# Kernel tuning notes

Measured on AMD Instinct MI355X. Metric: run time of the kernel, lower is better.

Reference implementation:

```python
import jax, jax.numpy as jnp
import numpy as np

N_NODES = 100000
N_EDGES = 1600000
D = 32  # atom and bond feature dim


def _mlp(x, W1, b1, W2, b2, W3, b3):
    # fff: Linear(in,128) -> ReLU -> Linear(128,64) -> ReLU -> Linear(64,32)
    h = jax.nn.relu(x @ W1 + b1)
    h = jax.nn.relu(h @ W2 + b2)
    return h @ W3 + b3


def _init_mlp(key, in_dim):
    ks = jax.random.split(key, 3)
    def lin(k, fan_in, fan_out):
        bound = 1.0 / np.sqrt(fan_in)
        kw, kb = jax.random.split(k)
        W = jax.random.uniform(kw, (fan_in, fan_out), jnp.float32, -bound, bound)
        b = jax.random.uniform(kb, (fan_out,), jnp.float32, -bound, bound)
        return W, b
    W1, b1 = lin(ks[0], in_dim, 128)
    W2, b2 = lin(ks[1], 128, 64)
    W3, b3 = lin(ks[2], 64, 32)
    return W1, b1, W2, b2, W3, b3


def setup_inputs() -> dict:
    key = jax.random.key(0)
    k_bonds, k_a1, k_a2, k_atoms, k_e, k_v = jax.random.split(key, 6)
    inp = {
        "bonds": jax.random.normal(k_bonds, (N_EDGES, D), jnp.float32),
        "bond_atom_1": jax.random.randint(k_a1, (N_EDGES,), 0, N_NODES, jnp.int64),
        "bond_atom_2": jax.random.randint(k_a2, (N_EDGES,), 0, N_NODES, jnp.int64),
        "atoms": jax.random.normal(k_atoms, (N_NODES, D), jnp.float32),
    }
    We1, be1, We2, be2, We3, be3 = _init_mlp(k_e, 96)
    Wv1, bv1, Wv2, bv2, Wv3, bv3 = _init_mlp(k_v, 64)
    inp.update(We1=We1, be1=be1, We2=We2, be2=be2, We3=We3, be3=be3,
               Wv1=Wv1, bv1=bv1, Wv2=Wv2, bv2=bv2, Wv3=Wv3, bv3=bv3)
    return inp


def reference(bonds, bond_atom_1, bond_atom_2, atoms,
              We1, be1, We2, be2, We3, be3,
              Wv1, bv1, Wv2, bv2, Wv3, bv3):
    # Edge update: gather endpoint atom features, concat with bond feats, MLP
    atom1 = atoms[bond_atom_1]                    # [E, D]
    atom2 = atoms[bond_atom_2]                    # [E, D]
    e_in = jnp.concatenate([atom1, atom2, bonds], axis=1)  # [E, 3D]
    new_bonds = _mlp(e_in, We1, be1, We2, be2, We3, be3)    # [E, 32]

    # Node update: scatter-mean new bond features onto target atoms
    # (PyG default flow aggregates messages at edge_index[1] == bond_atom_2)
    n = atoms.shape[0]
    seg_sum = jax.ops.segment_sum(new_bonds, bond_atom_2, num_segments=n)
    counts = jax.ops.segment_sum(jnp.ones((new_bonds.shape[0],), new_bonds.dtype),
                                 bond_atom_2, num_segments=n)
    mean_bonds = seg_sum / jnp.maximum(counts, 1.0)[:, None]  # [N, 32]

    v_in = jnp.concatenate([mean_bonds, atoms], axis=1)        # [N, 64]
    new_atoms = _mlp(v_in, Wv1, bv1, Wv2, bv2, Wv3, bv3)       # [N, 32]
    return (new_atoms, new_bonds)
```

## Files before the change

kernel.cpp:

```cpp
#include <hip/hip_runtime.h>
#include <hip/hip_bf16.h>

#define NN 100000
#define NE 1600000
#define NB_SCAN 391
#define ETILES 12500
#define EGRID 512
#define NGRID 1024

typedef __attribute__((ext_vector_type(8))) short bfrag8;
typedef __attribute__((ext_vector_type(4))) float f32x4;
typedef __attribute__((ext_vector_type(8))) unsigned short us8;
typedef __attribute__((ext_vector_type(4))) unsigned int u32x4;

__device__ __forceinline__ unsigned short f2bf(float f) {
  unsigned int u = __float_as_uint(f);
  u += 0x7fffu + ((u >> 16) & 1u);
  return (unsigned short)(u >> 16);
}

__device__ __forceinline__ unsigned int pk2(float a, float b) {
  unsigned int r;
  asm("v_cvt_pk_bf16_f32 %0, %1, %2" : "=v"(r) : "v"(a), "v"(b));
  return r;
}

__device__ __forceinline__ uint2 pk4(float v0, float v1, float v2, float v3) {
  return make_uint2(pk2(v0, v1), pk2(v2, v3));
}

__device__ __forceinline__ bfrag8 pack8(float4 a, float4 b) {
  union { u32x4 u; bfrag8 f; } c;
  c.u[0] = pk2(a.x, a.y); c.u[1] = pk2(a.z, a.w);
  c.u[2] = pk2(b.x, b.y); c.u[3] = pk2(b.z, b.w);
  return c.f;
}

__device__ __forceinline__ bfrag8 as_frag(us8 v) {
  union { us8 u; bfrag8 f; } c;
  c.u = v;
  return c.f;
}

__device__ __forceinline__ f32x4 mfma16(bfrag8 a, bfrag8 b, f32x4 c) {
  return __builtin_amdgcn_mfma_f32_16x16x32_bf16(a, b, c, 0, 0, 0);
}

__device__ __forceinline__ void gload_lds16(const void* g, void* l) {
  __builtin_amdgcn_global_load_lds(
      (const __attribute__((address_space(1))) unsigned int*)g,
      (__attribute__((address_space(3))) unsigned int*)l, 16, 0, 0);
}

__global__ void cvt_atoms(const float* __restrict__ src, unsigned short* __restrict__ dst) {
  int i = blockIdx.x * 256 + threadIdx.x;
  float4 v = *(const float4*)(src + (size_t)i * 4);
  *(uint2*)(dst + (size_t)i * 4) = pk4(v.x, v.y, v.z, v.w);
}

__global__ void pack_w(const float* __restrict__ src, unsigned short* __restrict__ dst,
                       int K, int N) {
  int i = blockIdx.x * 256 + threadIdx.x;
  if (i >= K * N) return;
  int j = i & 7;
  int gc = i >> 3;
  int c = gc % N;
  int g = gc / N;
  dst[i] = f2bf(src[(g * 8 + j) * N + c]);
}

__global__ void count_k(const int* __restrict__ a2, int* __restrict__ cnt) {
  int e = blockIdx.x * 256 + threadIdx.x;
  if (e < NE) atomicAdd(&cnt[a2[e]], 1);
}

__global__ void scan_blocks(const int* __restrict__ cnt, int* __restrict__ off,
                            int* __restrict__ bsum) {
  __shared__ int s[256];
  const int t = threadIdx.x;
  const int idx = blockIdx.x * 256 + t;
  int v = (idx < NN) ? cnt[idx] : 0;
  s[t] = v;
  __syncthreads();
  for (int d = 1; d < 256; d <<= 1) {
    int x = (t >= d) ? s[t - d] : 0;
    __syncthreads();
    s[t] += x;
    __syncthreads();
  }
  if (idx < NN) off[idx] = s[t] - v;
  if (t == 255) bsum[blockIdx.x] = s[255];
}

__global__ void scan_bsum(int* __restrict__ bsum) {
  __shared__ int s[512];
  const int t = threadIdx.x;
  int v = (t < NB_SCAN) ? bsum[t] : 0;
  s[t] = v;
  __syncthreads();
  for (int d = 1; d < 512; d <<= 1) {
    int x = (t >= d) ? s[t - d] : 0;
    __syncthreads();
    s[t] += x;
    __syncthreads();
  }
  if (t < NB_SCAN) bsum[t] = s[t] - v;
}

__global__ void scan_finalize(int* __restrict__ off, const int* __restrict__ bsum,
                              int* __restrict__ cursor) {
  int idx = blockIdx.x * 256 + threadIdx.x;
  if (idx < NN) {
    int o = off[idx] + bsum[blockIdx.x];
    off[idx] = o;
    cursor[idx] = o;
  }
  if (idx == 0) off[NN] = NE;
}

__global__ void fill_csr(const int* __restrict__ a2, int* __restrict__ cursor,
                         int* __restrict__ csr) {
  int e = blockIdx.x * 256 + threadIdx.x;
  if (e < NE) {
    int p = atomicAdd(&cursor[a2[e]], 1);
    csr[p] = e;
  }
}

__global__ __launch_bounds__(256, 2) void edge_kernel(
    const float* __restrict__ bonds, const int* __restrict__ a1p, const int* __restrict__ a2p,
    const unsigned short* __restrict__ atoms_bf,
    const float* __restrict__ be1, const float* __restrict__ be2, const float* __restrict__ be3,
    const unsigned short* __restrict__ wpack,
    float* __restrict__ new_bonds) {
  __shared__ unsigned short sW[22528];
  __shared__ float sB1[128], sB2[64], sB3[32];
  __shared__ unsigned short sH1[128 * 136];

  const int tid = threadIdx.x;
  const int lane = tid & 63, wv = tid >> 6;
  const int cl = lane & 15, q = lane >> 4;
  const int esub = wv * 32 + cl;

  {
    const char* src = (const char*)wpack;
    char* dst = (char*)sW;
#pragma unroll
    for (int i = 0; i < 11; ++i) {
      const int c = i * 4 + wv;
      gload_lds16(src + c * 1024 + lane * 16, dst + c * 1024);
    }
  }
  if (tid < 128) sB1[tid] = be1[tid];
  else if (tid < 192) sB2[tid - 128] = be2[tid - 128];
  else if (tid < 224) sB3[tid - 192] = be3[tid - 192];

  int tile = blockIdx.x;
  us8 ra1[2], ra2[2];
  float4 rb[2][2];
  int ia1n[2], ia2n[2];

#pragma unroll
  for (int t = 0; t < 2; ++t) {
    const int e = tile * 128 + esub + t * 16;
    const int ia1 = a1p[e], ia2 = a2p[e];
    ra1[t] = *(const us8*)(atoms_bf + (size_t)ia1 * 32 + q * 8);
    ra2[t] = *(const us8*)(atoms_bf + (size_t)ia2 * 32 + q * 8);
    const float* bp = bonds + (size_t)e * 32 + q * 8;
    rb[t][0] = *(const float4*)(bp);
    rb[t][1] = *(const float4*)(bp + 4);
  }
  {
    int tn = tile + EGRID; if (tn >= ETILES) tn = tile;
#pragma unroll
    for (int t = 0; t < 2; ++t) {
      const int e = tn * 128 + esub + t * 16;
      ia1n[t] = a1p[e]; ia2n[t] = a2p[e];
    }
  }
  __syncthreads();

  for (; tile < ETILES; tile += EGRID) {
    bfrag8 xb0[2], xb1[2], xb2[2];
#pragma unroll
    for (int t = 0; t < 2; ++t) {
      xb0[t] = as_frag(ra1[t]);
      xb1[t] = as_frag(ra2[t]);
      xb2[t] = pack8(rb[t][0], rb[t][1]);
    }
    const int tn = (tile + EGRID < ETILES) ? tile + EGRID : tile;
#pragma unroll
    for (int t = 0; t < 2; ++t) {
      ra1[t] = *(const us8*)(atoms_bf + (size_t)ia1n[t] * 32 + q * 8);
      ra2[t] = *(const us8*)(atoms_bf + (size_t)ia2n[t] * 32 + q * 8);
      const int e = tn * 128 + esub + t * 16;
      const float* bp = bonds + (size_t)e * 32 + q * 8;
      rb[t][0] = *(const float4*)(bp);
      rb[t][1] = *(const float4*)(bp + 4);
    }
    {
      int tnn = tile + 2 * EGRID; if (tnn >= ETILES) tnn = tn;
#pragma unroll
      for (int t = 0; t < 2; ++t) {
        const int e = tnn * 128 + esub + t * 16;
        ia1n[t] = a1p[e]; ia2n[t] = a2p[e];
      }
    }

#pragma unroll
    for (int rt = 0; rt < 8; ++rt) {
      const unsigned short* wa = &sW[(q * 128 + rt * 16 + cl) * 8];
      bfrag8 w0 = *(const bfrag8*)(wa);
      bfrag8 w1 = *(const bfrag8*)(wa + 4096);
      bfrag8 w2 = *(const bfrag8*)(wa + 8192);
      f32x4 acc[2];
      acc[0] = (f32x4){0.f, 0.f, 0.f, 0.f};
      acc[1] = (f32x4){0.f, 0.f, 0.f, 0.f};
#pragma unroll
      for (int t = 0; t < 2; ++t) {
        acc[t] = mfma16(w0, xb0[t], acc[t]);
        acc[t] = mfma16(w1, xb1[t], acc[t]);
        acc[t] = mfma16(w2, xb2[t], acc[t]);
      }
      const int c0 = rt * 16 + q * 4;
#pragma unroll
      for (int t = 0; t < 2; ++t) {
        uint2 hv = pk4(fmaxf(acc[t][0] + sB1[c0 + 0], 0.f),
                       fmaxf(acc[t][1] + sB1[c0 + 1], 0.f),
                       fmaxf(acc[t][2] + sB1[c0 + 2], 0.f),
                       fmaxf(acc[t][3] + sB1[c0 + 3], 0.f));
        *(uint2*)&sH1[(esub + t * 16) * 136 + c0] = hv;
      }
    }
    __syncthreads();

    bfrag8 hb[4][2];
#pragma unroll
    for (int t = 0; t < 2; ++t) {
      const unsigned short* hr = &sH1[(esub + t * 16) * 136 + q * 8];
#pragma unroll
      for (int ks = 0; ks < 4; ++ks) hb[ks][t] = *(const bfrag8*)(hr + ks * 32);
    }
    __syncthreads();

    unsigned short* sH2 = sH1;
#pragma unroll
    for (int rt = 0; rt < 4; ++rt) {
      f32x4 acc[2];
      acc[0] = (f32x4){0.f, 0.f, 0.f, 0.f};
      acc[1] = (f32x4){0.f, 0.f, 0.f, 0.f};
#pragma unroll
      for (int ks = 0; ks < 4; ++ks) {
        bfrag8 w = *(const bfrag8*)&sW[12288 + ks * 2048 + (q * 64 + rt * 16 + cl) * 8];
#pragma unroll
        for (int t = 0; t < 2; ++t) acc[t] = mfma16(w, hb[ks][t], acc[t]);
      }
      const int c0 = rt * 16 + q * 4;
#pragma unroll
      for (int t = 0; t < 2; ++t) {
        uint2 hv = pk4(fmaxf(acc[t][0] + sB2[c0 + 0], 0.f),
                       fmaxf(acc[t][1] + sB2[c0 + 1], 0.f),
                       fmaxf(acc[t][2] + sB2[c0 + 2], 0.f),
                       fmaxf(acc[t][3] + sB2[c0 + 3], 0.f));
        *(uint2*)&sH2[(esub + t * 16) * 72 + c0] = hv;
      }
    }
    __syncthreads();

    bfrag8 gb0[2], gb1[2];
#pragma unroll
    for (int t = 0; t < 2; ++t) {
      const unsigned short* hr = &sH2[(esub + t * 16) * 72 + q * 8];
      gb0[t] = *(const bfrag8*)(hr);
      gb1[t] = *(const bfrag8*)(hr + 32);
    }
#pragma unroll
    for (int rt = 0; rt < 2; ++rt) {
      bfrag8 w0 = *(const bfrag8*)&sW[20480 + (q * 32 + rt * 16 + cl) * 8];
      bfrag8 w1 = *(const bfrag8*)&sW[20480 + 1024 + (q * 32 + rt * 16 + cl) * 8];
      const int c0 = rt * 16 + q * 4;
#pragma unroll
      for (int t = 0; t < 2; ++t) {
        f32x4 acc = {0.f, 0.f, 0.f, 0.f};
        acc = mfma16(w0, gb0[t], acc);
        acc = mfma16(w1, gb1[t], acc);
        const int e = tile * 128 + esub + t * 16;
        float4 o;
        o.x = acc[0] + sB3[c0 + 0];
        o.y = acc[1] + sB3[c0 + 1];
        o.z = acc[2] + sB3[c0 + 2];
        o.w = acc[3] + sB3[c0 + 3];
        *(float4*)(new_bonds + (size_t)e * 32 + c0) = o;
      }
    }
    __syncthreads();
  }
}

__global__ __launch_bounds__(256, 4) void gather_mean(
    const int* __restrict__ off, const int* __restrict__ csr,
    const float* __restrict__ new_bonds, float* __restrict__ mean_f32) {
  const int tid = blockIdx.x * 256 + threadIdx.x;
  const int n = tid >> 3, sl = tid & 7;
  const int o0 = off[n], o1 = off[n + 1];
  float4 s0 = {0.f, 0.f, 0.f, 0.f}, s1 = {0.f, 0.f, 0.f, 0.f};
  int i = o0;
  for (; i + 1 < o1; i += 2) {
    const int ea = csr[i], eb = csr[i + 1];
    float4 a = *(const float4*)(new_bonds + (size_t)ea * 32 + sl * 4);
    float4 b = *(const float4*)(new_bonds + (size_t)eb * 32 + sl * 4);
    s0.x += a.x; s0.y += a.y; s0.z += a.z; s0.w += a.w;
    s1.x += b.x; s1.y += b.y; s1.z += b.z; s1.w += b.w;
  }
  if (i < o1) {
    const int ea = csr[i];
    float4 a = *(const float4*)(new_bonds + (size_t)ea * 32 + sl * 4);
    s0.x += a.x; s0.y += a.y; s0.z += a.z; s0.w += a.w;
  }
  const float inv = 1.0f / fmaxf((float)(o1 - o0), 1.0f);
  float4 m;
  m.x = (s0.x + s1.x) * inv;
  m.y = (s0.y + s1.y) * inv;
  m.z = (s0.z + s1.z) * inv;
  m.w = (s0.w + s1.w) * inv;
  *(float4*)(mean_f32 + (size_t)n * 32 + sl * 4) = m;
}

__global__ __launch_bounds__(256, 4) void node_mlp(
    const unsigned short* __restrict__ atoms_bf,
    const float* __restrict__ bv1, const float* __restrict__ bv2, const float* __restrict__ bv3,
    const unsigned short* __restrict__ wpack,
    const float* __restrict__ mean_f32, float* __restrict__ new_atoms) {
  __shared__ unsigned short sW[18432];
  __shared__ float sB1[128], sB2[64], sB3[32];
  __shared__ unsigned short sV[64 * 72];
  __shared__ unsigned short sH1[64 * 136];

  const int tid = threadIdx.x;
  const int lane = tid & 63, wv = tid >> 6;
  const int cl = lane & 15, q = lane >> 4;
  const int nl = tid >> 2, l4 = tid & 3;

  {
    const uint4* src = (const uint4*)wpack;
    uint4* dst = (uint4*)sW;
#pragma unroll
    for (int i = 0; i < 9; ++i) dst[tid + i * 256] = src[tid + i * 256];
  }
  if (tid < 128) sB1[tid] = bv1[tid];
  if (tid < 64) sB2[tid] = bv2[tid];
  if (tid < 32) sB3[tid] = bv3[tid];

  for (int n0 = blockIdx.x * 64; n0 < NN; n0 += NGRID * 64) {
    __syncthreads();

    {
      const int n = n0 + nl;
      if (n < NN) {
        if (l4 < 2) {
          const float* sp = mean_f32 + (size_t)n * 32 + l4 * 16;
          float4 a = *(const float4*)(sp);
          float4 b = *(const float4*)(sp + 4);
          float4 c = *(const float4*)(sp + 8);
          float4 d = *(const float4*)(sp + 12);
          uint4 o0, o1;
          o0.x = pk2(a.x, a.y); o0.y = pk2(a.z, a.w);
          o0.z = pk2(b.x, b.y); o0.w = pk2(b.z, b.w);
          o1.x = pk2(c.x, c.y); o1.y = pk2(c.z, c.w);
          o1.z = pk2(d.x, d.y); o1.w = pk2(d.z, d.w);
          *(uint4*)&sV[nl * 72 + l4 * 16] = o0;
          *(uint4*)&sV[nl * 72 + l4 * 16 + 8] = o1;
        } else {
          const unsigned short* ap = atoms_bf + (size_t)n * 32 + (l4 - 2) * 16;
          *(us8*)&sV[nl * 72 + 32 + (l4 - 2) * 16] = *(const us8*)(ap);
          *(us8*)&sV[nl * 72 + 32 + (l4 - 2) * 16 + 8] = *(const us8*)(ap + 8);
        }
      } else {
        us8 z = {0, 0, 0, 0, 0, 0, 0, 0};
        *(us8*)&sV[nl * 72 + l4 * 16] = z;
        *(us8*)&sV[nl * 72 + l4 * 16 + 8] = z;
      }
    }
    __syncthreads();

    const int nt = wv * 16;
    const int ng = n0 + nt + cl;

    bfrag8 vb0 = *(const bfrag8*)&sV[(nt + cl) * 72 + q * 8];
    bfrag8 vb1 = *(const bfrag8*)&sV[(nt + cl) * 72 + 32 + q * 8];
#pragma unroll
    for (int rt = 0; rt < 8; ++rt) {
      f32x4 acc = {0.f, 0.f, 0.f, 0.f};
      acc = mfma16(*(const bfrag8*)&sW[(q * 128 + rt * 16 + cl) * 8], vb0, acc);
      acc = mfma16(*(const bfrag8*)&sW[4096 + (q * 128 + rt * 16 + cl) * 8], vb1, acc);
      const int c0 = rt * 16 + q * 4;
      uint2 hv = pk4(fmaxf(acc[0] + sB1[c0 + 0], 0.f),
                     fmaxf(acc[1] + sB1[c0 + 1], 0.f),
                     fmaxf(acc[2] + sB1[c0 + 2], 0.f),
                     fmaxf(acc[3] + sB1[c0 + 3], 0.f));
      *(uint2*)&sH1[(nt + cl) * 136 + c0] = hv;
    }
    __syncthreads();

    bfrag8 hb[4];
    {
      const unsigned short* hr = &sH1[(nt + cl) * 136 + q * 8];
#pragma unroll
      for (int ks = 0; ks < 4; ++ks) hb[ks] = *(const bfrag8*)(hr + ks * 32);
    }
    __syncthreads();
#pragma unroll
    for (int rt = 0; rt < 4; ++rt) {
      f32x4 acc = {0.f, 0.f, 0.f, 0.f};
#pragma unroll
      for (int ks = 0; ks < 4; ++ks)
        acc = mfma16(*(const bfrag8*)&sW[8192 + ks * 2048 + (q * 64 + rt * 16 + cl) * 8], hb[ks], acc);
      const int c0 = rt * 16 + q * 4;
      uint2 hv = pk4(fmaxf(acc[0] + sB2[c0 + 0], 0.f),
                     fmaxf(acc[1] + sB2[c0 + 1], 0.f),
                     fmaxf(acc[2] + sB2[c0 + 2], 0.f),
                     fmaxf(acc[3] + sB2[c0 + 3], 0.f));
      *(uint2*)&sV[(nt + cl) * 72 + c0] = hv;
    }
    __syncthreads();

    bfrag8 gb0 = *(const bfrag8*)&sV[(nt + cl) * 72 + q * 8];
    bfrag8 gb1 = *(const bfrag8*)&sV[(nt + cl) * 72 + 32 + q * 8];
    if (ng < NN) {
      float* outp = new_atoms + (size_t)ng * 32;
#pragma unroll
      for (int rt = 0; rt < 2; ++rt) {
        f32x4 acc = {0.f, 0.f, 0.f, 0.f};
        acc = mfma16(*(const bfrag8*)&sW[16384 + (q * 32 + rt * 16 + cl) * 8], gb0, acc);
        acc = mfma16(*(const bfrag8*)&sW[16384 + 1024 + (q * 32 + rt * 16 + cl) * 8], gb1, acc);
        const int c0 = rt * 16 + q * 4;
        float4 o;
        o.x = acc[0] + sB3[c0 + 0];
        o.y = acc[1] + sB3[c0 + 1];
        o.z = acc[2] + sB3[c0 + 2];
        o.w = acc[3] + sB3[c0 + 3];
        *(float4*)(outp + c0) = o;
      }
    }
  }
}

extern "C" void kernel_launch(void* const* d_in, const int* in_sizes, int n_in,
                              void* d_out, int out_size, void* d_ws, size_t ws_size,
                              hipStream_t stream) {
  const float* bonds = (const float*)d_in[0];
  const int* a1 = (const int*)d_in[1];
  const int* a2 = (const int*)d_in[2];
  const float* atoms = (const float*)d_in[3];
  const float* We1 = (const float*)d_in[4];
  const float* be1 = (const float*)d_in[5];
  const float* We2 = (const float*)d_in[6];
  const float* be2 = (const float*)d_in[7];
  const float* We3 = (const float*)d_in[8];
  const float* be3 = (const float*)d_in[9];
  const float* Wv1 = (const float*)d_in[10];
  const float* bv1 = (const float*)d_in[11];
  const float* Wv2 = (const float*)d_in[12];
  const float* bv2 = (const float*)d_in[13];
  const float* Wv3 = (const float*)d_in[14];
  const float* bv3 = (const float*)d_in[15];

  float* out = (float*)d_out;
  float* new_atoms = out;
  float* new_bonds = out + (size_t)NN * 32;

  char* ws = (char*)d_ws;
  int* cnt    = (int*)(ws + 0);
  int* off    = (int*)(ws + 400000);
  int* bsum   = (int*)(ws + 800016);
  unsigned short* wp = (unsigned short*)(ws + 802064);
  int* csr    = (int*)(ws + 883984);
  unsigned short* atoms_bf = (unsigned short*)(ws + 7283984);

  hipMemsetAsync(cnt, 0, (size_t)NN * 4, stream);

  cvt_atoms<<<3125, 256, 0, stream>>>(atoms, atoms_bf);

  pack_w<<<48, 256, 0, stream>>>(We1, wp + 0, 96, 128);
  pack_w<<<32, 256, 0, stream>>>(We2, wp + 12288, 128, 64);
  pack_w<<<8, 256, 0, stream>>>(We3, wp + 20480, 64, 32);
  pack_w<<<32, 256, 0, stream>>>(Wv1, wp + 22528, 64, 128);
  pack_w<<<32, 256, 0, stream>>>(Wv2, wp + 30720, 128, 64);
  pack_w<<<8, 256, 0, stream>>>(Wv3, wp + 38912, 64, 32);

  count_k<<<(NE + 255) / 256, 256, 0, stream>>>(a2, cnt);
  scan_blocks<<<NB_SCAN, 256, 0, stream>>>(cnt, off, bsum);
  scan_bsum<<<1, 512, 0, stream>>>(bsum);
  scan_finalize<<<NB_SCAN, 256, 0, stream>>>(off, bsum, cnt);
  fill_csr<<<(NE + 255) / 256, 256, 0, stream>>>(a2, cnt, csr);

  edge_kernel<<<EGRID, 256, 0, stream>>>(bonds, a1, a2, atoms_bf, be1, be2, be3, wp,
                                         new_bonds);
  gather_mean<<<NN * 8 / 256, 256, 0, stream>>>(off, csr, new_bonds, new_atoms);
  node_mlp<<<NGRID, 256, 0, stream>>>(atoms_bf, bv1, bv2, bv3, wp + 22528,
                                      new_atoms , new_atoms );
}
```

Measured before the change: 428.3 us.

## Scatter bf16 edge outputs into CSR order and fuse prep kernels

The edge kernel now also writes a bf16 copy of each new bond row to its CSR-sorted position, so the mean aggregation reads contiguous bf16 rows per node instead of gathering fp32 rows at random. The mean is stored in bf16 and loaded directly by the node MLP. The atom convert, weight packing and count kernels are merged into one launch, and the single-block bsum scan is folded into scan_finalize. This adds an extra scattered 2-byte write stream in the edge kernel and rounds the aggregation inputs to bf16. The fast path only runs when the workspace is large enough.

New measurement: 394.7 us. -7.9%, faster.

```diff
diff --git a/kernel.cpp b/kernel.cpp
--- a/kernel.cpp
+++ b/kernel.cpp
@@ -42,6 +42,9 @@
   return c.f;
 }
 
+__device__ __forceinline__ float bl(unsigned int u) { return __uint_as_float(u << 16); }
+__device__ __forceinline__ float bh(unsigned int u) { return __uint_as_float(u & 0xffff0000u); }
+
 __device__ __forceinline__ f32x4 mfma16(bfrag8 a, bfrag8 b, f32x4 c) {
   return __builtin_amdgcn_mfma_f32_16x16x32_bf16(a, b, c, 0, 0, 0);
 }
@@ -52,26 +55,35 @@
       (__attribute__((address_space(3))) unsigned int*)l, 16, 0, 0);
 }
 
-__global__ void cvt_atoms(const float* __restrict__ src, unsigned short* __restrict__ dst) {
-  int i = blockIdx.x * 256 + threadIdx.x;
-  float4 v = *(const float4*)(src + (size_t)i * 4);
-  *(uint2*)(dst + (size_t)i * 4) = pk4(v.x, v.y, v.z, v.w);
-}
-
-__global__ void pack_w(const float* __restrict__ src, unsigned short* __restrict__ dst,
-                       int K, int N) {
-  int i = blockIdx.x * 256 + threadIdx.x;
-  if (i >= K * N) return;
-  int j = i & 7;
-  int gc = i >> 3;
-  int c = gc % N;
-  int g = gc / N;
-  dst[i] = f2bf(src[(g * 8 + j) * N + c]);
-}
-
-__global__ void count_k(const int* __restrict__ a2, int* __restrict__ cnt) {
-  int e = blockIdx.x * 256 + threadIdx.x;
-  if (e < NE) atomicAdd(&cnt[a2[e]], 1);
+__global__ void prep(const float* __restrict__ atoms, unsigned short* __restrict__ atoms_bf,
+                     const int* __restrict__ a2, int* __restrict__ cnt,
+                     const float* __restrict__ We1, const float* __restrict__ We2,
+                     const float* __restrict__ We3, const float* __restrict__ Wv1,
+                     const float* __restrict__ Wv2, const float* __restrict__ Wv3,
+                     unsigned short* __restrict__ wp) {
+  const int b = blockIdx.x, tid = threadIdx.x;
+  if (b < 3125) {
+    const int i = b * 256 + tid;
+    float4 v = *(const float4*)(atoms + (size_t)i * 4);
+    *(uint2*)(atoms_bf + (size_t)i * 4) = pk4(v.x, v.y, v.z, v.w);
+  } else if (b < 3125 + 6250) {
+    const int e = (b - 3125) * 256 + tid;
+    if (e < NE) atomicAdd(&cnt[a2[e]], 1);
+  } else {
+    const int i = (b - 9375) * 256 + tid;
+    const float* src; int base, K, N;
+    if (i < 12288)      { src = We1; base = 0;     K = 96;  N = 128; }
+    else if (i < 20480) { src = We2; base = 12288; K = 128; N = 64;  }
+    else if (i < 22528) { src = We3; base = 20480; K = 64;  N = 32;  }
+    else if (i < 30720) { src = Wv1; base = 22528; K = 64;  N = 128; }
+    else if (i < 38912) { src = Wv2; base = 30720; K = 128; N = 64;  }
+    else                { src = Wv3; base = 38912; K = 64;  N = 32;  }
+    const int il = i - base;
+    const int j = il & 7, gc = il >> 3;
+    const int c = gc % N, g = gc / N;
+    wp[i] = f2bf(src[(g * 8 + j) * N + c]);
+    (void)K;
+  }
 }
 
 __global__ void scan_blocks(const int* __restrict__ cnt, int* __restrict__ off,
@@ -92,38 +104,35 @@
   if (t == 255) bsum[blockIdx.x] = s[255];
 }
 
-__global__ void scan_bsum(int* __restrict__ bsum) {
-  __shared__ int s[512];
-  const int t = threadIdx.x;
-  int v = (t < NB_SCAN) ? bsum[t] : 0;
-  s[t] = v;
-  __syncthreads();
-  for (int d = 1; d < 512; d <<= 1) {
-    int x = (t >= d) ? s[t - d] : 0;
-    __syncthreads();
-    s[t] += x;
-    __syncthreads();
-  }
-  if (t < NB_SCAN) bsum[t] = s[t] - v;
-}
-
 __global__ void scan_finalize(int* __restrict__ off, const int* __restrict__ bsum,
                               int* __restrict__ cursor) {
-  int idx = blockIdx.x * 256 + threadIdx.x;
+  __shared__ int red[256];
+  const int b = blockIdx.x, t = threadIdx.x;
+  int s = 0;
+  for (int k = t; k < b; k += 256) s += bsum[k];
+  red[t] = s;
+  __syncthreads();
+  for (int d = 128; d > 0; d >>= 1) {
+    if (t < d) red[t] += red[t + d];
+    __syncthreads();
+  }
+  const int base = red[0];
+  const int idx = b * 256 + t;
   if (idx < NN) {
-    int o = off[idx] + bsum[blockIdx.x];
+    int o = off[idx] + base;
     off[idx] = o;
     cursor[idx] = o;
   }
   if (idx == 0) off[NN] = NE;
 }
 
-__global__ void fill_csr(const int* __restrict__ a2, int* __restrict__ cursor,
-                         int* __restrict__ csr) {
+__global__ void fill_k(const int* __restrict__ a2, int* __restrict__ cursor,
+                       int* __restrict__ buf, int mode) {
   int e = blockIdx.x * 256 + threadIdx.x;
   if (e < NE) {
     int p = atomicAdd(&cursor[a2[e]], 1);
-    csr[p] = e;
+    if (mode) buf[e] = p;
+    else buf[p] = e;
   }
 }
 
@@ -132,7 +141,8 @@
     const unsigned short* __restrict__ atoms_bf,
     const float* __restrict__ be1, const float* __restrict__ be2, const float* __restrict__ be3,
     const unsigned short* __restrict__ wpack,
-    float* __restrict__ new_bonds) {
+    float* __restrict__ new_bonds,
+    const int* __restrict__ pos, unsigned short* __restrict__ nb_bf) {
   __shared__ unsigned short sW[22528];
   __shared__ float sB1[128], sB2[64], sB3[32];
   __shared__ unsigned short sH1[128 * 136];
@@ -187,6 +197,11 @@
       xb0[t] = as_frag(ra1[t]);
       xb1[t] = as_frag(ra2[t]);
       xb2[t] = pack8(rb[t][0], rb[t][1]);
+    }
+    int posc[2] = {0, 0};
+    if (nb_bf) {
+#pragma unroll
+      for (int t = 0; t < 2; ++t) posc[t] = pos[tile * 128 + esub + t * 16];
     }
     const int tn = (tile + EGRID < ETILES) ? tile + EGRID : tile;
 #pragma unroll
@@ -291,13 +306,43 @@
         o.z = acc[2] + sB3[c0 + 2];
         o.w = acc[3] + sB3[c0 + 3];
         *(float4*)(new_bonds + (size_t)e * 32 + c0) = o;
-      }
-    }
-    __syncthreads();
-  }
-}
-
-__global__ __launch_bounds__(256, 4) void gather_mean(
+        if (nb_bf) {
+          *(uint2*)(nb_bf + (size_t)posc[t] * 32 + c0) =
+              make_uint2(pk2(o.x, o.y), pk2(o.z, o.w));
+        }
+      }
+    }
+    __syncthreads();
+  }
+}
+
+__global__ __launch_bounds__(256, 8) void gather_seq(
+    const int* __restrict__ off, const unsigned short* __restrict__ nb_bf,
+    unsigned short* __restrict__ mean_bf) {
+  const int gt = blockIdx.x * 256 + threadIdx.x;
+  const int n = gt >> 3, sl = gt & 7;
+  const int o0 = off[n], o1 = off[n + 1];
+  const int deg = o1 - o0;
+  float s0 = 0.f, s1 = 0.f, s2 = 0.f, s3 = 0.f;
+  const unsigned short* p = nb_bf + (size_t)o0 * 32 + sl * 4;
+  int i = 0;
+  for (; i + 1 < deg; i += 2) {
+    uint2 a = *(const uint2*)(p);
+    uint2 b = *(const uint2*)(p + 32);
+    p += 64;
+    s0 += bl(a.x) + bl(b.x); s1 += bh(a.x) + bh(b.x);
+    s2 += bl(a.y) + bl(b.y); s3 += bh(a.y) + bh(b.y);
+  }
+  if (i < deg) {
+    uint2 a = *(const uint2*)(p);
+    s0 += bl(a.x); s1 += bh(a.x); s2 += bl(a.y); s3 += bh(a.y);
+  }
+  const float inv = 1.0f / fmaxf((float)deg, 1.0f);
+  *(uint2*)(mean_bf + (size_t)n * 32 + sl * 4) =
+      make_uint2(pk2(s0 * inv, s1 * inv), pk2(s2 * inv, s3 * inv));
+}
+
+__global__ __launch_bounds__(256, 8) void gather_rand(
     const int* __restrict__ off, const int* __restrict__ csr,
     const float* __restrict__ new_bonds, float* __restrict__ mean_f32) {
   const int tid = blockIdx.x * 256 + threadIdx.x;
@@ -326,11 +371,12 @@
   *(float4*)(mean_f32 + (size_t)n * 32 + sl * 4) = m;
 }
 
+template <int MODE>
 __global__ __launch_bounds__(256, 4) void node_mlp(
     const unsigned short* __restrict__ atoms_bf,
     const float* __restrict__ bv1, const float* __restrict__ bv2, const float* __restrict__ bv3,
     const unsigned short* __restrict__ wpack,
-    const float* __restrict__ mean_f32, float* __restrict__ new_atoms) {
+    const void* __restrict__ mean_src, float* __restrict__ new_atoms) {
   __shared__ unsigned short sW[18432];
   __shared__ float sB1[128], sB2[64], sB3[32];
   __shared__ unsigned short sV[64 * 72];
@@ -358,18 +404,24 @@
       const int n = n0 + nl;
       if (n < NN) {
         if (l4 < 2) {
-          const float* sp = mean_f32 + (size_t)n * 32 + l4 * 16;
-          float4 a = *(const float4*)(sp);
-          float4 b = *(const float4*)(sp + 4);
-          float4 c = *(const float4*)(sp + 8);
-          float4 d = *(const float4*)(sp + 12);
-          uint4 o0, o1;
-          o0.x = pk2(a.x, a.y); o0.y = pk2(a.z, a.w);
-          o0.z = pk2(b.x, b.y); o0.w = pk2(b.z, b.w);
-          o1.x = pk2(c.x, c.y); o1.y = pk2(c.z, c.w);
-          o1.z = pk2(d.x, d.y); o1.w = pk2(d.z, d.w);
-          *(uint4*)&sV[nl * 72 + l4 * 16] = o0;
-          *(uint4*)&sV[nl * 72 + l4 * 16 + 8] = o1;
+          if (MODE == 1) {
+            const unsigned short* mp = (const unsigned short*)mean_src + (size_t)n * 32 + l4 * 16;
+            *(us8*)&sV[nl * 72 + l4 * 16] = *(const us8*)(mp);
+            *(us8*)&sV[nl * 72 + l4 * 16 + 8] = *(const us8*)(mp + 8);
+          } else {
+            const float* sp = (const float*)mean_src + (size_t)n * 32 + l4 * 16;
+            float4 a = *(const float4*)(sp);
+            float4 b = *(const float4*)(sp + 4);
+            float4 c = *(const float4*)(sp + 8);
+            float4 d = *(const float4*)(sp + 12);
+            uint4 o0, o1;
+            o0.x = pk2(a.x, a.y); o0.y = pk2(a.z, a.w);
+            o0.z = pk2(b.x, b.y); o0.w = pk2(b.z, b.w);
+            o1.x = pk2(c.x, c.y); o1.y = pk2(c.z, c.w);
+            o1.z = pk2(d.x, d.y); o1.w = pk2(d.z, d.w);
+            *(uint4*)&sV[nl * 72 + l4 * 16] = o0;
+            *(uint4*)&sV[nl * 72 + l4 * 16 + 8] = o1;
+          }
         } else {
           const unsigned short* ap = atoms_bf + (size_t)n * 32 + (l4 - 2) * 16;
           *(us8*)&sV[nl * 72 + 32 + (l4 - 2) * 16] = *(const us8*)(ap);
@@ -474,29 +526,32 @@
   int* off    = (int*)(ws + 400000);
   int* bsum   = (int*)(ws + 800016);
   unsigned short* wp = (unsigned short*)(ws + 802064);
-  int* csr    = (int*)(ws + 883984);
+  int* poscsr = (int*)(ws + 883984);
   unsigned short* atoms_bf = (unsigned short*)(ws + 7283984);
+  unsigned short* mean_bf  = (unsigned short*)(ws + 13683984);
+  unsigned short* nb_bf    = (unsigned short*)(ws + 20083984);
+
+  const int fast = (ws_size >= (size_t)122483984) ? 1 : 0;
 
   hipMemsetAsync(cnt, 0, (size_t)NN * 4, stream);
 
-  cvt_atoms<<<3125, 256, 0, stream>>>(atoms, atoms_bf);
-
-  pack_w<<<48, 256, 0, stream>>>(We1, wp + 0, 96, 128);
-  pack_w<<<32, 256, 0, stream>>>(We2, wp + 12288, 128, 64);
-  pack_w<<<8, 256, 0, stream>>>(We3, wp + 20480, 64, 32);
-  pack_w<<<32, 256, 0, stream>>>(Wv1, wp + 22528, 64, 128);
-  pack_w<<<32, 256, 0, stream>>>(Wv2, wp + 30720, 128, 64);
-  pack_w<<<8, 256, 0, stream>>>(Wv3, wp + 38912, 64, 32);
-
-  count_k<<<(NE + 255) / 256, 256, 0, stream>>>(a2, cnt);
+  prep<<<9535, 256, 0, stream>>>(atoms, atoms_bf, a2, cnt,
+                                 We1, We2, We3, Wv1, Wv2, Wv3, wp);
+
   scan_blocks<<<NB_SCAN, 256, 0, stream>>>(cnt, off, bsum);
-  scan_bsum<<<1, 512, 0, stream>>>(bsum);
   scan_finalize<<<NB_SCAN, 256, 0, stream>>>(off, bsum, cnt);
-  fill_csr<<<(NE + 255) / 256, 256, 0, stream>>>(a2, cnt, csr);
+  fill_k<<<(NE + 255) / 256, 256, 0, stream>>>(a2, cnt, poscsr, fast);
 
   edge_kernel<<<EGRID, 256, 0, stream>>>(bonds, a1, a2, atoms_bf, be1, be2, be3, wp,
-                                         new_bonds);
-  gather_mean<<<NN * 8 / 256, 256, 0, stream>>>(off, csr, new_bonds, new_atoms);
-  node_mlp<<<NGRID, 256, 0, stream>>>(atoms_bf, bv1, bv2, bv3, wp + 22528,
-                                      new_atoms , new_atoms );
-}
+                                         new_bonds, poscsr, fast ? nb_bf : nullptr);
+
+  if (fast) {
+    gather_seq<<<NN * 8 / 256, 256, 0, stream>>>(off, nb_bf, mean_bf);
+    node_mlp<1><<<NGRID, 256, 0, stream>>>(atoms_bf, bv1, bv2, bv3, wp + 22528,
+                                           mean_bf, new_atoms);
+  } else {
+    gather_rand<<<NN * 8 / 256, 256, 0, stream>>>(off, poscsr, new_bonds, new_atoms);
+    node_mlp<0><<<NGRID, 256, 0, stream>>>(atoms_bf, bv1, bv2, bv3, wp + 22528,
+                                           new_atoms, new_atoms);
+  }
+}
```
